# Performance work log

Measured on AMD Instinct MI355X. Metric: run time of the kernel, lower is better.

The kernel has to match this reference:

```python
import jax, jax.numpy as jnp
import numpy as np

IN, HID, RANK, B = 2048, 2048, 512, 8192


def setup_inputs() -> dict:
    key = jax.random.key(0)
    ks = jax.random.split(key, 16)
    s_in = 1.0 / np.sqrt(IN + HID)
    s_r = 1.0 / np.sqrt(RANK)
    inp = {
        "x": jax.random.normal(ks[0], (B, IN), jnp.float32),
        "h": jax.random.normal(ks[1], (B, HID), jnp.float32),
        "c": jax.random.normal(ks[2], (B, HID), jnp.float32),
    }
    names = ["i", "f", "c", "o"]
    for idx, g in enumerate(names):
        inp[f"U{g}"] = jax.random.uniform(ks[3 + 3 * idx], (IN + HID, RANK), jnp.float32, -s_in, s_in)
        inp[f"V{g}"] = jax.random.uniform(ks[4 + 3 * idx], (RANK, HID), jnp.float32, -s_r, s_r)
        inp[f"b{g}"] = jnp.zeros((HID,), jnp.float32)
    return inp


def reference(x, h, c, Ui, Vi, bi, Uf, Vf, bf, Uc, Vc, bc, Uo, Vo, bo):
    combined = jnp.concatenate([x, h], axis=1)  # [B, IN+HID]

    def gate(U, V, b):
        return (combined @ U) @ V + b  # low-rank: [B,R] then [B,HID]

    i = jax.nn.sigmoid(gate(Ui, Vi, bi))
    f = jax.nn.sigmoid(gate(Uf, Vf, bf))
    o = jax.nn.sigmoid(gate(Uo, Vo, bo))
    c_hat = jnp.tanh(gate(Uc, Vc, bc))
    c_new = f * c + i * c_hat
    h_new = o * jnp.tanh(c_new)
    return (h_new, c_new)
```

## Files before the change

### kernel.cpp

```cpp
#include <hip/hip_runtime.h>
#include <hip/hip_bf16.h>
#include <cstdint>
#include <cstddef>

typedef __bf16 bf16;
typedef __bf16 bf16x8 __attribute__((ext_vector_type(8)));
typedef float f32x4 __attribute__((ext_vector_type(4)));

#define BATCH 8192
#define IN_DIM 2048
#define HID 2048
#define RANK 512
#define KDIM 4096
#define NG 2048


__device__ __forceinline__ void gload16(const void* g, void* l) {
  __builtin_amdgcn_global_load_lds(
      (const __attribute__((address_space(1))) unsigned int*)g,
      (__attribute__((address_space(3))) unsigned int*)l, 16, 0, 0);
}

__device__ __forceinline__ float sigmoidf_(float x) {
  return 1.0f / (1.0f + __expf(-x));
}
__device__ __forceinline__ float tanhf_(float x) {
  return 1.0f - 2.0f / (__expf(2.0f * x) + 1.0f);
}

#define GBAR  __builtin_amdgcn_s_barrier()
#define VMC0  asm volatile("s_waitcnt vmcnt(0)" ::: "memory")
#define VMC2  asm volatile("s_waitcnt vmcnt(2)" ::: "memory")
#define VMC4  asm volatile("s_waitcnt vmcnt(4)" ::: "memory")
#define VMC8  asm volatile("s_waitcnt vmcnt(8)" ::: "memory")
#define SB0   __builtin_amdgcn_sched_barrier(0)
#define LGKMC(N) do { asm volatile("s_waitcnt lgkmcnt(" #N ")" ::: "memory"); SB0; } while (0)

__device__ __forceinline__ void stage_half(const bf16* __restrict__ g0, int ld,
                                           int row0, int kcol, bf16* lbase, int tid) {
  const int wid = tid >> 6;
  #pragma unroll
  for (int q = 0; q < 2; ++q) {
    const int slot = q * 512 + tid;
    const int row = slot >> 3, cb = slot & 7;
    const int gcb = cb ^ (row & 7);
    gload16(g0 + (size_t)(row0 + row) * ld + kcol + gcb * 8,
            lbase + (size_t)(q * 64 + wid * 8) * 64);
  }
}

#define LD_Bp(PB)                                                              \
  _Pragma("unroll") for (int j = 0; j < 4; ++j)                                \
  _Pragma("unroll") for (int ks = 0; ks < 2; ++ks)                             \
    b[j][ks] = *(const bf16x8*)((PB) + (wn + j * 16 + lr) * 64                 \
                                 + ((((ks << 2) | lk) ^ sw) << 3));


#define LD_APAR(PA, Q, P)                                                      \
  _Pragma("unroll") for (int ai = 0; ai < 2; ++ai)                             \
  _Pragma("unroll") for (int ks = 0; ks < 2; ++ks)                             \
    a[P][ai][ks] = *(const bf16x8*)((PA) + (wm + (Q) * 32 + ai * 16 + lr) * 64 \
                                 + ((((ks << 2) | lk) ^ sw) << 3));

#define MFMAQP(Q, P)                                                           \
  _Pragma("unroll") for (int ai = 0; ai < 2; ++ai)                             \
  _Pragma("unroll") for (int ks = 0; ks < 2; ++ks)                             \
  _Pragma("unroll") for (int j = 0; j < 4; ++j)                                \
    acc[(Q) * 2 + ai][j] = __builtin_amdgcn_mfma_f32_16x16x32_bf16(            \
        a[P][ai][ks], b[j][ks], acc[(Q) * 2 + ai][j], 0, 0, 0);

template <int NT>
__device__ __forceinline__ void gemm_core(const bf16* __restrict__ A, int lda, int m0,
                                          const bf16* __restrict__ B, int ldb, int n0,
                                          bf16* lds, f32x4 (&acc)[8][4]) {
  const int tid = threadIdx.x;
  const int wid = tid >> 6, lane = tid & 63;
  const int wm = (wid >> 2) * 128, wn = (wid & 3) * 64;
  const int lr = lane & 15, lk = lane >> 4;
  const int sw = lr & 7;
  bf16x8 a[2][2][2];
  bf16x8 b[4][2];

  bf16* Ab0 = lds;
  bf16* Ab1 = lds + 16384;
  bf16* Rg0 = lds + 2 * 16384;
  bf16* Rg1 = lds + 3 * 16384;
  bf16* Rg2 = lds + 4 * 16384;

  #pragma unroll
  for (int i = 0; i < 8; ++i)
    #pragma unroll
    for (int j = 0; j < 4; ++j) acc[i][j] = (f32x4){0.f, 0.f, 0.f, 0.f};

  stage_half(A, lda, m0,       0,   Ab0,        tid);
  stage_half(A, lda, m0 + 128, 0,   Ab0 + 8192, tid);
  stage_half(B, ldb, n0,       0,   Rg0,        tid);
  stage_half(B, ldb, n0 + 128, 0,   Rg0 + 8192, tid);
  stage_half(B, ldb, n0,       64,  Rg1,        tid);
  stage_half(B, ldb, n0 + 128, 64,  Rg1 + 8192, tid);
  stage_half(B, ldb, n0,       128, Rg2,        tid);
  stage_half(B, ldb, n0 + 128, 128, Rg2 + 8192, tid);
  VMC8;
  GBAR;
  LD_Bp(Rg0);
  SB0;

  bf16 *pBc = Rg0, *pBn = Rg1, *pBn2 = Rg2;
  bf16 *pAc = Ab0, *pAa = Ab1;
  for (int c = 0; c < NT; ++c) {
    const int kc1 = ((c + 1) & (NT - 1)) * 64;
    const int kc3 = ((c + 3) & (NT - 1)) * 64;
    LD_APAR(pAc, 0, 0); LD_APAR(pAc, 1, 1); SB0;
    stage_half(A, lda, m0,       kc1, pAa,        tid); SB0;
    GBAR;
    LGKMC(4);
    __builtin_amdgcn_s_setprio(1); MFMAQP(0, 0); __builtin_amdgcn_s_setprio(0);
    LD_APAR(pAc, 2, 0); SB0;
    stage_half(A, lda, m0 + 128, kc1, pAa + 8192, tid); SB0;
    GBAR;
    LGKMC(4);
    __builtin_amdgcn_s_setprio(1); MFMAQP(1, 1); __builtin_amdgcn_s_setprio(0);
    LD_APAR(pAc, 3, 1); SB0;
    stage_half(B, ldb, n0,       kc3, pBc,        tid); SB0;
    GBAR;
    LGKMC(4);
    __builtin_amdgcn_s_setprio(1); MFMAQP(2, 0); __builtin_amdgcn_s_setprio(0);
    stage_half(B, ldb, n0 + 128, kc3, pBc + 8192, tid); SB0;
    VMC4;
    GBAR;
    LGKMC(0);
    __builtin_amdgcn_s_setprio(1); MFMAQP(3, 1); __builtin_amdgcn_s_setprio(0);
    LD_Bp(pBn);
    SB0;
    bf16* tt = pBc; pBc = pBn; pBn = pBn2; pBn2 = tt;
    tt = pAc; pAc = pAa; pAa = tt;
  }
}


#define LD_AP(PA, Q, P)                                                        \
  _Pragma("unroll") for (int ks = 0; ks < 2; ++ks)                             \
    ap[P][ks] = *(const bf16x8*)((PA) + (wm + (Q) * 16 + lr) * 64              \
                                 + ((((ks << 2) | lk) ^ sw) << 3));

#define MFMAP(Q, P)                                                            \
  _Pragma("unroll") for (int ks = 0; ks < 2; ++ks)                             \
  _Pragma("unroll") for (int j = 0; j < 4; ++j)                                \
    acc[(Q)][j] = __builtin_amdgcn_mfma_f32_16x16x32_bf16(                     \
        ap[P][ks], b[j][ks], acc[(Q)][j], 0, 0, 0);

template <int NT>
__device__ __forceinline__ void gemm_coreP(const bf16* __restrict__ A, int lda, int m0,
                                           const bf16* __restrict__ B, int ldb, int n0,
                                           bf16* lds, f32x4 (&acc)[4][4]) {
  const int tid = threadIdx.x;
  const int wid = tid >> 6, lane = tid & 63;
  const int wm = (wid >> 1) * 64, wn = (wid & 1) * 64;
  const int lr = lane & 15, lk = lane >> 4;
  const int sw = lr & 7;
  bf16x8 ap[2][2], b[4][2];

  bf16* Ab0 = lds;
  bf16* Ab1 = lds + 16384;
  bf16* Rg0 = lds + 32768;
  bf16* Rg1 = lds + 40960;
  bf16* Rg2 = lds + 49152;

  #pragma unroll
  for (int i = 0; i < 4; ++i)
    #pragma unroll
    for (int j = 0; j < 4; ++j) acc[i][j] = (f32x4){0.f, 0.f, 0.f, 0.f};

  stage_half(A, lda, m0,       0,   Ab0,        tid);
  stage_half(A, lda, m0 + 128, 0,   Ab0 + 8192, tid);
  stage_half(B, ldb, n0, 0,   Rg0, tid);
  stage_half(B, ldb, n0, 64,  Rg1, tid);
  stage_half(B, ldb, n0, 128, Rg2, tid);
  VMC4;
  GBAR;
  LD_Bp(Rg0);
  SB0;

  bf16 *pBc = Rg0, *pBn = Rg1, *pBn2 = Rg2;
  bf16 *pAc = Ab0, *pAa = Ab1;
  for (int c = 0; c < NT; ++c) {
    const int kc1 = ((c + 1) & (NT - 1)) * 64;
    const int kc3 = ((c + 3) & (NT - 1)) * 64;
    LD_AP(pAc, 0, 0); LD_AP(pAc, 1, 1); SB0;
    stage_half(A, lda, m0,       kc1, pAa,        tid); SB0;
    GBAR;
    LGKMC(2);
    __builtin_amdgcn_s_setprio(1); MFMAP(0, 0); __builtin_amdgcn_s_setprio(0);
    LD_AP(pAc, 2, 0); SB0;
    stage_half(A, lda, m0 + 128, kc1, pAa + 8192, tid); SB0;
    GBAR;
    LGKMC(2);
    __builtin_amdgcn_s_setprio(1); MFMAP(1, 1); __builtin_amdgcn_s_setprio(0);
    LD_AP(pAc, 3, 1); SB0;
    stage_half(B, ldb, n0, kc3, pBc, tid); SB0;
    GBAR;
    LGKMC(2);
    __builtin_amdgcn_s_setprio(1); MFMAP(2, 0); __builtin_amdgcn_s_setprio(0);
    VMC2;
    LGKMC(0);
    GBAR;
    __builtin_amdgcn_s_setprio(1); MFMAP(3, 1); __builtin_amdgcn_s_setprio(0);
    LD_Bp(pBn);
    SB0;
    bf16* tt = pBc; pBc = pBn; pBn = pBn2; pBn2 = tt;
    tt = pAc; pAc = pAa; pAa = tt;
  }
}


__global__ void k_convert_combined(const float* __restrict__ x,
                                   const float* __restrict__ h,
                                   bf16* __restrict__ out) {
  size_t i4 = (size_t)blockIdx.x * blockDim.x + threadIdx.x;
  size_t base = i4 * 4;
  int col = (int)(base & (KDIM - 1));
  size_t row = base >> 12;
  const float* src = (col < IN_DIM) ? (x + row * IN_DIM + col)
                                    : (h + row * (size_t)HID + (col - IN_DIM));
  float4 v = *(const float4*)src;
  union { bf16 b[4]; uint2 u; } p;
  p.b[0] = (bf16)v.x; p.b[1] = (bf16)v.y; p.b[2] = (bf16)v.z; p.b[3] = (bf16)v.w;
  *(uint2*)(out + base) = p.u;
}


__global__ void k_tconv4(const float* __restrict__ s0, const float* __restrict__ s1,
                         const float* __restrict__ s2, const float* __restrict__ s3,
                         bf16* __restrict__ out, int nrow, int ncol,
                         long ostride, long gstride) {
  __shared__ float t[32][33];
  const float* in = blockIdx.z == 0 ? s0 : blockIdx.z == 1 ? s1
                  : blockIdx.z == 2 ? s2 : s3;
  bf16* o = out + (size_t)blockIdx.z * gstride;
  int c0 = blockIdx.x * 32, r0 = blockIdx.y * 32;
  int tx = threadIdx.x, ty = threadIdx.y;
  #pragma unroll
  for (int yy = ty; yy < 32; yy += 8)
    t[yy][tx] = in[(size_t)(r0 + yy) * ncol + c0 + tx];
  __syncthreads();
  #pragma unroll
  for (int yy = ty; yy < 32; yy += 8)
    o[(size_t)(c0 + yy) * ostride + r0 + tx] = (bf16)t[tx][yy];
}


__launch_bounds__(512, 2)
__global__ void k_gemm1(const bf16* __restrict__ A,
                        const bf16* __restrict__ Bt,
                        bf16* __restrict__ R) {
  __shared__ __align__(16) bf16 lds[81920];
  const int bx = blockIdx.x;
  const int id = (bx & 7) * 32 + (bx >> 3);
  const int m0 = (id >> 3) * 256, n0 = (id & 7) * 256;
  f32x4 acc[8][4];
  gemm_core<KDIM / 64>(A, KDIM, m0, Bt, KDIM, n0, lds, acc);

  const int tid = threadIdx.x;
  const int wid = tid >> 6, lane = tid & 63;
  const int wm = (wid >> 2) * 128, wn = (wid & 3) * 64;
  const int lr = lane & 15, lk = lane >> 4;
  #pragma unroll
  for (int i = 0; i < 8; ++i)
    #pragma unroll
    for (int j = 0; j < 4; ++j)
      #pragma unroll
      for (int v = 0; v < 4; ++v)
        R[(size_t)(m0 + wm + i * 16 + lk * 4 + v) * NG + (n0 + wn + j * 16 + lr)] =
            (bf16)acc[i][j][v];
}


__launch_bounds__(512, 2)
__global__ void k_pair_ic(const bf16* __restrict__ Rb,
                          const bf16* __restrict__ Vt,
                          const float* __restrict__ bi, const float* __restrict__ bc,
                          bf16* __restrict__ sv) {
  __shared__ __align__(16) bf16 lds[57344];
  const int bx = blockIdx.x;
  const int id = (bx & 7) * 64 + (bx >> 3);
  const int m0 = (id >> 4) * 256, n0 = (id & 15) * 128;

  f32x4 accI[4][4], accC[4][4];
  gemm_coreP<RANK / 64>(Rb + 0 * RANK, NG, m0,
                        Vt + (size_t)0 * HID * RANK, RANK, n0, lds, accI);
  VMC0;
  GBAR;
  gemm_coreP<RANK / 64>(Rb + 2 * RANK, NG, m0,
                        Vt + (size_t)2 * HID * RANK, RANK, n0, lds, accC);

  const int tid = threadIdx.x;
  const int wid = tid >> 6, lane = tid & 63;
  const int wm = (wid >> 1) * 64, wn = (wid & 1) * 64;
  const int lr = lane & 15, lk = lane >> 4;
  #pragma unroll
  for (int j = 0; j < 4; ++j) {
    const int col = n0 + wn + j * 16 + lr;
    const float bji = bi[col], bjc = bc[col];
    #pragma unroll
    for (int q = 0; q < 4; ++q)
      #pragma unroll
      for (int v = 0; v < 4; ++v) {
        const int row = m0 + wm + q * 16 + lk * 4 + v;
        const float s = sigmoidf_(accI[q][j][v] + bji) * tanhf_(accC[q][j][v] + bjc);
        sv[(size_t)row * HID + col] = (bf16)s;
      }
  }
}


__launch_bounds__(512, 2)
__global__ void k_pair_fo(const bf16* __restrict__ Rb,
                          const bf16* __restrict__ Vt,
                          const float* __restrict__ bf_, const float* __restrict__ bo,
                          const bf16* __restrict__ sv,
                          const float* __restrict__ cin,
                          float* __restrict__ hout, float* __restrict__ cout) {
  __shared__ __align__(16) bf16 lds[57344];
  const int bx = blockIdx.x;
  const int id = (bx & 7) * 64 + (bx >> 3);
  const int m0 = (id >> 4) * 256, n0 = (id & 15) * 128;

  f32x4 accF[4][4], accO[4][4];
  gemm_coreP<RANK / 64>(Rb + 1 * RANK, NG, m0,
                        Vt + (size_t)1 * HID * RANK, RANK, n0, lds, accF);
  VMC0;
  GBAR;
  gemm_coreP<RANK / 64>(Rb + 3 * RANK, NG, m0,
                        Vt + (size_t)3 * HID * RANK, RANK, n0, lds, accO);

  const int tid = threadIdx.x;
  const int wid = tid >> 6, lane = tid & 63;
  const int wm = (wid >> 1) * 64, wn = (wid & 1) * 64;
  const int lr = lane & 15, lk = lane >> 4;
  #pragma unroll
  for (int j = 0; j < 4; ++j) {
    const int col = n0 + wn + j * 16 + lr;
    const float bjf = bf_[col], bjo = bo[col];
    #pragma unroll
    for (int q = 0; q < 4; ++q)
      #pragma unroll
      for (int v = 0; v < 4; ++v) {
        const int row = m0 + wm + q * 16 + lk * 4 + v;
        const size_t e = (size_t)row * HID + col;
        const float f = sigmoidf_(accF[q][j][v] + bjf);
        const float cn = f * cin[e] + (float)sv[e];
        cout[e] = cn;
        hout[e] = sigmoidf_(accO[q][j][v] + bjo) * tanhf_(cn);
      }
  }
}


extern "C" void kernel_launch(void* const* d_in, const int* in_sizes, int n_in,
                              void* d_out, int out_size, void* d_ws, size_t ws_size,
                              hipStream_t stream) {
  const float* x = (const float*)d_in[0];
  const float* h = (const float*)d_in[1];
  const float* c = (const float*)d_in[2];
  const float* U[4] = {(const float*)d_in[3], (const float*)d_in[6],
                       (const float*)d_in[9], (const float*)d_in[12]};
  const float* V[4] = {(const float*)d_in[4], (const float*)d_in[7],
                       (const float*)d_in[10], (const float*)d_in[13]};
  const float* b[4] = {(const float*)d_in[5], (const float*)d_in[8],
                       (const float*)d_in[11], (const float*)d_in[14]};

  char* ws = (char*)d_ws;
  bf16* combined = (bf16*)ws;
  bf16* Ut       = (bf16*)(ws + 67108864);
  bf16* Vt       = (bf16*)(ws + 67108864 + 16777216);
  bf16* Rbuf     = (bf16*)(ws + 67108864 + 16777216 + 8388608);
  bf16* sv       = (bf16*)ws;

  float* hout = (float*)d_out;
  float* cout = hout + (size_t)BATCH * HID;

  k_convert_combined<<<(BATCH * (size_t)KDIM / 4) / 256, 256, 0, stream>>>(x, h, combined);

  k_tconv4<<<dim3(RANK / 32, KDIM / 32, 4), dim3(32, 8), 0, stream>>>(
      U[0], U[1], U[2], U[3], Ut, KDIM, RANK, KDIM, (long)RANK * KDIM);
  k_tconv4<<<dim3(HID / 32, RANK / 32, 4), dim3(32, 8), 0, stream>>>(
      V[0], V[1], V[2], V[3], Vt, RANK, HID, RANK, (long)HID * RANK);

  k_gemm1<<<256, 512, 0, stream>>>(combined, Ut, Rbuf);

  k_pair_ic<<<512, 512, 0, stream>>>(Rbuf, Vt, b[0], b[2], sv);
  k_pair_fo<<<512, 512, 0, stream>>>(Rbuf, Vt, b[1], b[3], sv, c, hout, cout);
}
```

Measured before the change: 332.3 us.

## Interleave paired gate GEMMs in one pipeline and vectorize weight transpose

The two back-to-back second-stage GEMMs in each pair kernel become one software pipeline that alternates k-steps between the two gates. The B-tile ring then continuously prefetches the other gate's V slices, which removes the full drain (vmcnt(0) plus barrier) and the pipeline refill between the two GEMMs. Separately, the weight transpose-convert kernel moves to 64x64 tiles with float4 loads and 16-byte bf16 stores. The interleaved schedule makes the A-operand loads switch column offsets every step, and its correctness depends on the prefetch indices lining up.

```diff
diff --git a/kernel.cpp b/kernel.cpp
--- a/kernel.cpp
+++ b/kernel.cpp
@@ -29,7 +29,6 @@
 }
 
 #define GBAR  __builtin_amdgcn_s_barrier()
-#define VMC0  asm volatile("s_waitcnt vmcnt(0)" ::: "memory")
 #define VMC2  asm volatile("s_waitcnt vmcnt(2)" ::: "memory")
 #define VMC4  asm volatile("s_waitcnt vmcnt(4)" ::: "memory")
 #define VMC8  asm volatile("s_waitcnt vmcnt(8)" ::: "memory")
@@ -143,16 +142,44 @@
     ap[P][ks] = *(const bf16x8*)((PA) + (wm + (Q) * 16 + lr) * 64              \
                                  + ((((ks << 2) | lk) ^ sw) << 3));
 
-#define MFMAP(Q, P)                                                            \
+#define MFMAP2(ACC, Q, P)                                                      \
   _Pragma("unroll") for (int ks = 0; ks < 2; ++ks)                             \
   _Pragma("unroll") for (int j = 0; j < 4; ++j)                                \
-    acc[(Q)][j] = __builtin_amdgcn_mfma_f32_16x16x32_bf16(                     \
-        ap[P][ks], b[j][ks], acc[(Q)][j], 0, 0, 0);
+    ACC[(Q)][j] = __builtin_amdgcn_mfma_f32_16x16x32_bf16(                     \
+        ap[P][ks], b[j][ks], ACC[(Q)][j], 0, 0, 0);
+
+#define STEP2(ACC, ACOL, BPTR, BCOL)                                           \
+  {                                                                            \
+    LD_AP(pAc, 0, 0); LD_AP(pAc, 1, 1); SB0;                                   \
+    stage_half(Rb, lda, m0,       (ACOL), pAa,        tid); SB0;               \
+    GBAR;                                                                      \
+    LGKMC(2);                                                                  \
+    __builtin_amdgcn_s_setprio(1); MFMAP2(ACC, 0, 0); __builtin_amdgcn_s_setprio(0); \
+    LD_AP(pAc, 2, 0); SB0;                                                     \
+    stage_half(Rb, lda, m0 + 128, (ACOL), pAa + 8192, tid); SB0;               \
+    GBAR;                                                                      \
+    LGKMC(2);                                                                  \
+    __builtin_amdgcn_s_setprio(1); MFMAP2(ACC, 1, 1); __builtin_amdgcn_s_setprio(0); \
+    LD_AP(pAc, 3, 1); SB0;                                                     \
+    stage_half((BPTR), ldb, n0, (BCOL), pBc, tid); SB0;                        \
+    GBAR;                                                                      \
+    LGKMC(2);                                                                  \
+    __builtin_amdgcn_s_setprio(1); MFMAP2(ACC, 2, 0); __builtin_amdgcn_s_setprio(0); \
+    VMC2;                                                                      \
+    LGKMC(0);                                                                  \
+    GBAR;                                                                      \
+    __builtin_amdgcn_s_setprio(1); MFMAP2(ACC, 3, 1); __builtin_amdgcn_s_setprio(0); \
+    LD_Bp(pBn);                                                                \
+    SB0;                                                                       \
+    bf16* tt_ = pBc; pBc = pBn; pBn = pBn2; pBn2 = tt_;                        \
+    tt_ = pAc; pAc = pAa; pAa = tt_;                                           \
+  }
 
 template <int NT>
-__device__ __forceinline__ void gemm_coreP(const bf16* __restrict__ A, int lda, int m0,
-                                           const bf16* __restrict__ B, int ldb, int n0,
-                                           bf16* lds, f32x4 (&acc)[4][4]) {
+__device__ __forceinline__ void gemm_coreP2(
+    const bf16* __restrict__ Rb, int lda, int m0, int kgA, int kgB,
+    const bf16* __restrict__ VA, const bf16* __restrict__ VB, int ldb, int n0,
+    bf16* lds, f32x4 (&accA)[4][4], f32x4 (&accB)[4][4]) {
   const int tid = threadIdx.x;
   const int wid = tid >> 6, lane = tid & 63;
   const int wm = (wid >> 1) * 64, wn = (wid & 1) * 64;
@@ -169,13 +196,16 @@
   #pragma unroll
   for (int i = 0; i < 4; ++i)
     #pragma unroll
-    for (int j = 0; j < 4; ++j) acc[i][j] = (f32x4){0.f, 0.f, 0.f, 0.f};
-
-  stage_half(A, lda, m0,       0,   Ab0,        tid);
-  stage_half(A, lda, m0 + 128, 0,   Ab0 + 8192, tid);
-  stage_half(B, ldb, n0, 0,   Rg0, tid);
-  stage_half(B, ldb, n0, 64,  Rg1, tid);
-  stage_half(B, ldb, n0, 128, Rg2, tid);
+    for (int j = 0; j < 4; ++j) {
+      accA[i][j] = (f32x4){0.f, 0.f, 0.f, 0.f};
+      accB[i][j] = (f32x4){0.f, 0.f, 0.f, 0.f};
+    }
+
+  stage_half(Rb, lda, m0,       kgA, Ab0,        tid);
+  stage_half(Rb, lda, m0 + 128, kgA, Ab0 + 8192, tid);
+  stage_half(VA, ldb, n0, 0,  Rg0, tid);
+  stage_half(VB, ldb, n0, 0,  Rg1, tid);
+  stage_half(VA, ldb, n0, 64, Rg2, tid);
   VMC4;
   GBAR;
   LD_Bp(Rg0);
@@ -183,32 +213,9 @@
 
   bf16 *pBc = Rg0, *pBn = Rg1, *pBn2 = Rg2;
   bf16 *pAc = Ab0, *pAa = Ab1;
-  for (int c = 0; c < NT; ++c) {
-    const int kc1 = ((c + 1) & (NT - 1)) * 64;
-    const int kc3 = ((c + 3) & (NT - 1)) * 64;
-    LD_AP(pAc, 0, 0); LD_AP(pAc, 1, 1); SB0;
-    stage_half(A, lda, m0,       kc1, pAa,        tid); SB0;
-    GBAR;
-    LGKMC(2);
-    __builtin_amdgcn_s_setprio(1); MFMAP(0, 0); __builtin_amdgcn_s_setprio(0);
-    LD_AP(pAc, 2, 0); SB0;
-    stage_half(A, lda, m0 + 128, kc1, pAa + 8192, tid); SB0;
-    GBAR;
-    LGKMC(2);
-    __builtin_amdgcn_s_setprio(1); MFMAP(1, 1); __builtin_amdgcn_s_setprio(0);
-    LD_AP(pAc, 3, 1); SB0;
-    stage_half(B, ldb, n0, kc3, pBc, tid); SB0;
-    GBAR;
-    LGKMC(2);
-    __builtin_amdgcn_s_setprio(1); MFMAP(2, 0); __builtin_amdgcn_s_setprio(0);
-    VMC2;
-    LGKMC(0);
-    GBAR;
-    __builtin_amdgcn_s_setprio(1); MFMAP(3, 1); __builtin_amdgcn_s_setprio(0);
-    LD_Bp(pBn);
-    SB0;
-    bf16* tt = pBc; pBc = pBn; pBn = pBn2; pBn2 = tt;
-    tt = pAc; pAc = pAa; pAa = tt;
+  for (int t = 0; t < NT; ++t) {
+    STEP2(accA, kgB + t * 64, VB, ((t + 1) & (NT - 1)) * 64);
+    STEP2(accB, kgA + ((t + 1) & (NT - 1)) * 64, VA, ((t + 2) & (NT - 1)) * 64);
   }
 }
 
@@ -229,23 +236,40 @@
 }
 
 
-__global__ void k_tconv4(const float* __restrict__ s0, const float* __restrict__ s1,
-                         const float* __restrict__ s2, const float* __restrict__ s3,
-                         bf16* __restrict__ out, int nrow, int ncol,
-                         long ostride, long gstride) {
-  __shared__ float t[32][33];
+__global__ void k_tconv4v(const float* __restrict__ s0, const float* __restrict__ s1,
+                          const float* __restrict__ s2, const float* __restrict__ s3,
+                          bf16* __restrict__ out, int nrow, int ncol,
+                          long ostride, long gstride) {
+  __shared__ float t[64][65];
   const float* in = blockIdx.z == 0 ? s0 : blockIdx.z == 1 ? s1
                   : blockIdx.z == 2 ? s2 : s3;
   bf16* o = out + (size_t)blockIdx.z * gstride;
-  int c0 = blockIdx.x * 32, r0 = blockIdx.y * 32;
-  int tx = threadIdx.x, ty = threadIdx.y;
-  #pragma unroll
-  for (int yy = ty; yy < 32; yy += 8)
-    t[yy][tx] = in[(size_t)(r0 + yy) * ncol + c0 + tx];
+  const int c0 = blockIdx.x * 64, r0 = blockIdx.y * 64;
+  const int tid = threadIdx.x;
+
+  {
+    const int rb = tid >> 4;
+    const int cq = (tid & 15) * 4;
+    #pragma unroll
+    for (int i = 0; i < 4; ++i) {
+      const int rr = rb + i * 16;
+      float4 v = *(const float4*)(in + (size_t)(r0 + rr) * ncol + c0 + cq);
+      t[rr][cq] = v.x; t[rr][cq + 1] = v.y; t[rr][cq + 2] = v.z; t[rr][cq + 3] = v.w;
+    }
+  }
   __syncthreads();
-  #pragma unroll
-  for (int yy = ty; yy < 32; yy += 8)
-    o[(size_t)(c0 + yy) * ostride + r0 + tx] = (bf16)t[tx][yy];
+  {
+    const int orow = tid >> 2;
+    const int cb = (tid & 3) * 16;
+    union { bf16 hh[8]; uint4 u; } p0, p1;
+    #pragma unroll
+    for (int k = 0; k < 8; ++k) p0.hh[k] = (bf16)t[cb + k][orow];
+    #pragma unroll
+    for (int k = 0; k < 8; ++k) p1.hh[k] = (bf16)t[cb + 8 + k][orow];
+    bf16* ob = o + (size_t)(c0 + orow) * ostride + r0 + cb;
+    *(uint4*)ob = p0.u;
+    *(uint4*)(ob + 8) = p1.u;
+  }
 }
 
 
@@ -286,12 +310,9 @@
   const int m0 = (id >> 4) * 256, n0 = (id & 15) * 128;
 
   f32x4 accI[4][4], accC[4][4];
-  gemm_coreP<RANK / 64>(Rb + 0 * RANK, NG, m0,
-                        Vt + (size_t)0 * HID * RANK, RANK, n0, lds, accI);
-  VMC0;
-  GBAR;
-  gemm_coreP<RANK / 64>(Rb + 2 * RANK, NG, m0,
-                        Vt + (size_t)2 * HID * RANK, RANK, n0, lds, accC);
+  gemm_coreP2<RANK / 64>(Rb, NG, m0, 0 * RANK, 2 * RANK,
+                         Vt + (size_t)0 * HID * RANK, Vt + (size_t)2 * HID * RANK,
+                         RANK, n0, lds, accI, accC);
 
   const int tid = threadIdx.x;
   const int wid = tid >> 6, lane = tid & 63;
@@ -326,12 +347,9 @@
   const int m0 = (id >> 4) * 256, n0 = (id & 15) * 128;
 
   f32x4 accF[4][4], accO[4][4];
-  gemm_coreP<RANK / 64>(Rb + 1 * RANK, NG, m0,
-                        Vt + (size_t)1 * HID * RANK, RANK, n0, lds, accF);
-  VMC0;
-  GBAR;
-  gemm_coreP<RANK / 64>(Rb + 3 * RANK, NG, m0,
-                        Vt + (size_t)3 * HID * RANK, RANK, n0, lds, accO);
+  gemm_coreP2<RANK / 64>(Rb, NG, m0, 1 * RANK, 3 * RANK,
+                         Vt + (size_t)1 * HID * RANK, Vt + (size_t)3 * HID * RANK,
+                         RANK, n0, lds, accF, accO);
 
   const int tid = threadIdx.x;
   const int wid = tid >> 6, lane = tid & 63;
@@ -381,9 +399,9 @@
 
   k_convert_combined<<<(BATCH * (size_t)KDIM / 4) / 256, 256, 0, stream>>>(x, h, combined);
 
-  k_tconv4<<<dim3(RANK / 32, KDIM / 32, 4), dim3(32, 8), 0, stream>>>(
+  k_tconv4v<<<dim3(RANK / 64, KDIM / 64, 4), 256, 0, stream>>>(
       U[0], U[1], U[2], U[3], Ut, KDIM, RANK, KDIM, (long)RANK * KDIM);
-  k_tconv4<<<dim3(HID / 32, RANK / 32, 4), dim3(32, 8), 0, stream>>>(
+  k_tconv4v<<<dim3(HID / 64, RANK / 64, 4), 256, 0, stream>>>(
       V[0], V[1], V[2], V[3], Vt, RANK, HID, RANK, (long)HID * RANK);
 
   k_gemm1<<<256, 512, 0, stream>>>(combined, Ut, Rbuf);
```

Result: faster. 320.0 us (median of 2 runs) (-3.7%).
